# Kernel optimization log

Measured on AMD Instinct MI355X. Metric: run time of the kernel, lower is better.

## Reference

```python
import jax, jax.numpy as jnp
import numpy as np

B, T, C = 2, 2048, 1024
NH = 16

def setup_inputs() -> dict:
    key = jax.random.key(0)
    ks = jax.random.split(key, 5)
    s = 0.02
    return {
        "x": jax.random.normal(ks[0], (B, T, C), dtype=jnp.float32),
        "w_attn": jax.random.normal(ks[1], (C, 3 * C), dtype=jnp.float32) * s,
        "b_attn": jax.random.normal(ks[2], (3 * C,), dtype=jnp.float32) * s,
        "w_proj": jax.random.normal(ks[3], (C, C), dtype=jnp.float32) * s,
        "b_proj": jax.random.normal(ks[4], (C,), dtype=jnp.float32) * s,
        "n_heads": NH,
    }

def reference(x, w_attn, b_attn, w_proj, b_proj, n_heads):
    Bx, Tx, Cx = x.shape
    hd = Cx // n_heads
    qkv = x @ w_attn + b_attn                      # [B,T,3C]
    q, k, v = jnp.split(qkv, 3, axis=-1)
    # [B,T,H,hd] -> [B,H,T,hd]
    q = q.reshape(Bx, Tx, n_heads, hd).transpose(0, 2, 1, 3)
    k = k.reshape(Bx, Tx, n_heads, hd).transpose(0, 2, 1, 3)
    v = v.reshape(Bx, Tx, n_heads, hd).transpose(0, 2, 1, 3)
    scale = 1.0 / np.sqrt(hd).astype(np.float32)
    att = jnp.einsum('bhqd,bhkd->bhqk', q, k) * scale   # [B,H,T,T]
    causal = jnp.tril(jnp.ones((Tx, Tx), dtype=bool))
    att = jnp.where(causal[None, None], att, -jnp.inf)
    att = jax.nn.softmax(att, axis=-1)
    y = jnp.einsum('bhqk,bhkd->bhqd', att, v)            # [B,H,T,hd]
    y = y.transpose(0, 2, 1, 3).reshape(Bx, Tx, Cx)
    return y @ w_proj + b_proj
```

## Files before the change

### kernel.cpp

```cpp
#include <hip/hip_runtime.h>

typedef __bf16 bf16x8 __attribute__((ext_vector_type(8)));
typedef __bf16 bf16x4 __attribute__((ext_vector_type(4)));
typedef float  f32x4  __attribute__((ext_vector_type(4)));

#define MFMA_BF16(a, b, c) __builtin_amdgcn_mfma_f32_16x16x32_bf16((a), (b), (c), 0, 0, 0)
#define NEG_INF (-1e30f)
#define SCL 0.18033688f

__device__ __forceinline__ void gld16(const void* g, void* l) {
  __builtin_amdgcn_global_load_lds(
      (const __attribute__((address_space(1))) void*)g,
      (__attribute__((address_space(3))) void*)l, 16, 0, 0);
}

__global__ void cast_f32_bf16(const float* __restrict__ in,
                              __bf16* __restrict__ out, int n) {
  int i = (blockIdx.x * 256 + threadIdx.x) * 8;
  if (i >= n) return;
  float4 a = *(const float4*)&in[i];
  float4 b = *(const float4*)&in[i + 4];
  bf16x8 v;
  v[0] = (__bf16)a.x; v[1] = (__bf16)a.y; v[2] = (__bf16)a.z; v[3] = (__bf16)a.w;
  v[4] = (__bf16)b.x; v[5] = (__bf16)b.y; v[6] = (__bf16)b.z; v[7] = (__bf16)b.w;
  *(bf16x8*)&out[i] = v;
}

__global__ void transpose_f32_bf16(const float* __restrict__ in,
                                   __bf16* __restrict__ out, int R, int C) {
  __shared__ float t[32][33];
  int tx = threadIdx.x & 31, ty = threadIdx.x >> 5;
  int x = blockIdx.x * 32 + tx;
  int y0 = blockIdx.y * 32 + ty;
#pragma unroll
  for (int i = 0; i < 4; ++i)
    t[ty + 8 * i][tx] = in[(size_t)(y0 + 8 * i) * C + x];
  __syncthreads();
  int x2 = blockIdx.y * 32 + tx;
#pragma unroll
  for (int i = 0; i < 4; ++i)
    out[(size_t)(blockIdx.x * 32 + ty + 8 * i) * R + x2] = (__bf16)t[tx][ty + 8 * i];
}

__global__ void transpose_v(const __bf16* __restrict__ qkv,
                            __bf16* __restrict__ vt) {
  __shared__ __bf16 t[32][33];
  int tx = threadIdx.x & 31, ty = threadIdx.x >> 5;
  int bh = blockIdx.z, b = bh >> 4, h = bh & 15;
  int t0 = blockIdx.x * 32, d0 = blockIdx.y * 32;
#pragma unroll
  for (int i = 0; i < 4; ++i)
    t[ty + 8 * i][tx] =
        qkv[(size_t)(b * 2048 + t0 + ty + 8 * i) * 3072 + 2048 + h * 64 + d0 + tx];
  __syncthreads();
#pragma unroll
  for (int i = 0; i < 4; ++i)
    vt[(size_t)(bh * 64 + d0 + ty + 8 * i) * 2048 + t0 + tx] = t[tx][ty + 8 * i];
}

#define BN 128
#define BK 64

template <int BMT, typename TC>
__global__ __launch_bounds__(256) void gemm_bt_bias(
    const __bf16* __restrict__ A, const __bf16* __restrict__ Bt,
    const float* __restrict__ bias, TC* __restrict__ Cmat,
    int M, int N, int K) {
  constexpr int NI = BMT / 32;
  __shared__ __align__(16) __bf16 As[BMT * BK];
  __shared__ __align__(16) __bf16 Bs[BN * BK];
  int tid = threadIdx.x;
  int wave = tid >> 6, lane = tid & 63;
  int l16 = lane & 15, quad = lane >> 4;
  int wm = wave >> 1, wn = wave & 1;
  int m0 = blockIdx.y * BMT, n0 = blockIdx.x * BN;

  f32x4 acc[NI][4];
#pragma unroll
  for (int i = 0; i < NI; ++i)
#pragma unroll
    for (int j = 0; j < 4; ++j) acc[i][j] = (f32x4){0.f, 0.f, 0.f, 0.f};

  int row = tid >> 3;
  int kc = ((tid & 7) ^ ((tid >> 3) & 7)) * 8;
  int xr = (l16 & 7) * 8;

  for (int k0 = 0; k0 < K; k0 += BK) {
#pragma unroll
    for (int i = 0; i < NI; ++i)
      gld16(&A[(size_t)(m0 + row + i * 32) * K + k0 + kc],
            (char*)As + (i * 256 + wave * 64) * 16);
#pragma unroll
    for (int j = 0; j < 4; ++j)
      gld16(&Bt[(size_t)(n0 + row + j * 32) * K + k0 + kc],
            (char*)Bs + (j * 256 + wave * 64) * 16);
    __syncthreads();
#pragma unroll
    for (int ks = 0; ks < 2; ++ks) {
      bf16x8 af[NI], bfr[4];
#pragma unroll
      for (int i = 0; i < NI; ++i)
        af[i] = *(const bf16x8*)&As[(wm * (BMT / 2) + i * 16 + l16) * BK +
                                    ((ks * 32 + quad * 8) ^ xr)];
#pragma unroll
      for (int j = 0; j < 4; ++j)
        bfr[j] = *(const bf16x8*)&Bs[(wn * 64 + j * 16 + l16) * BK +
                                     ((ks * 32 + quad * 8) ^ xr)];
#pragma unroll
      for (int i = 0; i < NI; ++i)
#pragma unroll
        for (int j = 0; j < 4; ++j) acc[i][j] = MFMA_BF16(af[i], bfr[j], acc[i][j]);
    }
    __syncthreads();
  }
#pragma unroll
  for (int i = 0; i < NI; ++i) {
#pragma unroll
    for (int j = 0; j < 4; ++j) {
      int col = n0 + wn * 64 + j * 16 + l16;
      float bv = bias[col];
#pragma unroll
      for (int r = 0; r < 4; ++r) {
        int rw = m0 + wm * (BMT / 2) + i * 16 + quad * 4 + r;
        Cmat[(size_t)rw * N + col] = (TC)(acc[i][j][r] + bv);
      }
    }
  }
}

__global__ __launch_bounds__(256) void attn_causal(
    const __bf16* __restrict__ qkv, const __bf16* __restrict__ vt,
    __bf16* __restrict__ y) {
  __shared__ __align__(16) __bf16 Kb[2][64 * 64];
  __shared__ __align__(16) __bf16 Vb[2][64 * 64];
  __shared__ __align__(16) __bf16 Ps[4][16 * 72];
  const int tid = threadIdx.x;
  const int wave = tid >> 6, lane = tid & 63;
  const int l16 = lane & 15, quad = lane >> 4;
  const int bh = blockIdx.x;
  const int b = bh >> 4, h = bh & 15;
  const int RS = 3072;

  const int row0 = tid >> 3;
  const int kcs = ((tid & 7) ^ ((tid >> 3) & 7)) * 8;
  const int xr = (l16 & 7) * 8;
  const __bf16* kbase = qkv + (size_t)(b * 2048) * RS + 1024 + h * 64 + kcs;
  const __bf16* vbase = vt + (size_t)(bh * 64) * 2048 + kcs;

#pragma unroll 1
  for (int phase = 0; phase < 2; ++phase) {
    const int qt = phase ? (31 - (int)blockIdx.y) : (int)blockIdx.y;

    int qrow = b * 2048 + qt * 64 + wave * 16 + l16;
    const __bf16* qbase = qkv + (size_t)qrow * RS + h * 64;
    bf16x8 qf0 = *(const bf16x8*)(qbase + quad * 8);
    bf16x8 qf1 = *(const bf16x8*)(qbase + 32 + quad * 8);

    float l_i = 0.f;
    f32x4 o[4];
#pragma unroll
    for (int j = 0; j < 4; ++j) o[j] = (f32x4){0.f, 0.f, 0.f, 0.f};

#pragma unroll
    for (int i = 0; i < 2; ++i) {
      gld16(kbase + (size_t)(row0 + 32 * i) * RS,
            (char*)Kb[0] + (i * 256 + tid) * 16);
      gld16(vbase + (size_t)(row0 + 32 * i) * 2048,
            (char*)Vb[0] + (i * 256 + tid) * 16);
    }
    __syncthreads();

    for (int kt = 0; kt <= qt; ++kt) {
      const int cur = kt & 1;
      if (kt < qt) {
#pragma unroll
        for (int i = 0; i < 2; ++i) {
          gld16(kbase + (size_t)((kt + 1) * 64 + row0 + 32 * i) * RS,
                (char*)Kb[cur ^ 1] + (i * 256 + tid) * 16);
          gld16(vbase + (size_t)(row0 + 32 * i) * 2048 + (kt + 1) * 64,
                (char*)Vb[cur ^ 1] + (i * 256 + tid) * 16);
        }
      }

      f32x4 s[4];
#pragma unroll
      for (int j = 0; j < 4; ++j) s[j] = (f32x4){0.f, 0.f, 0.f, 0.f};
#pragma unroll
      for (int j = 0; j < 4; ++j) {
        bf16x8 kf0 = *(const bf16x8*)&Kb[cur][(j * 16 + l16) * 64 + ((quad * 8) ^ xr)];
        bf16x8 kf1 = *(const bf16x8*)&Kb[cur][(j * 16 + l16) * 64 + ((32 + quad * 8) ^ xr)];
        s[j] = MFMA_BF16(kf0, qf0, s[j]);
        s[j] = MFMA_BF16(kf1, qf1, s[j]);
      }

      if (kt == qt) {
        int qg = wave * 16 + l16;
#pragma unroll
        for (int j = 0; j < 4; ++j)
#pragma unroll
          for (int r = 0; r < 4; ++r)
            if (j * 16 + quad * 4 + r > qg) s[j][r] = NEG_INF;
      }

#pragma unroll
      for (int j = 0; j < 4; ++j) {
        bf16x4 pb;
#pragma unroll
        for (int r = 0; r < 4; ++r) {
          float p = __builtin_amdgcn_exp2f(s[j][r] * SCL);
          l_i += p;
          pb[r] = (__bf16)p;
        }
        *(bf16x4*)&Ps[wave][l16 * 72 + j * 16 + quad * 4] = pb;
      }

#pragma unroll
      for (int ks = 0; ks < 2; ++ks) {
        bf16x8 pf = *(const bf16x8*)&Ps[wave][l16 * 72 + ks * 32 + quad * 8];
#pragma unroll
        for (int j = 0; j < 4; ++j) {
          bf16x8 vf = *(const bf16x8*)&Vb[cur][(j * 16 + l16) * 64 +
                                              ((ks * 32 + quad * 8) ^ xr)];
          o[j] = MFMA_BF16(pf, vf, o[j]);
        }
      }
      __syncthreads();
    }

    float lred = l_i;
    lred += __shfl_xor(lred, 16);
    lred += __shfl_xor(lred, 32);
    int orow = b * 2048 + qt * 64 + wave * 16 + quad * 4;
#pragma unroll
    for (int r = 0; r < 4; ++r) {
      float inv = 1.f / __shfl(lred, quad * 4 + r);
#pragma unroll
      for (int j = 0; j < 4; ++j)
        y[(size_t)(orow + r) * 1024 + h * 64 + j * 16 + l16] = (__bf16)(o[j][r] * inv);
    }
  }
}

extern "C" void kernel_launch(void* const* d_in, const int* in_sizes, int n_in,
                              void* d_out, int out_size, void* d_ws, size_t ws_size,
                              hipStream_t stream) {
  (void)in_sizes; (void)n_in; (void)out_size; (void)ws_size;
  const float* x      = (const float*)d_in[0];
  const float* w_attn = (const float*)d_in[1];
  const float* b_attn = (const float*)d_in[2];
  const float* w_proj = (const float*)d_in[3];
  const float* b_proj = (const float*)d_in[4];
  float* out = (float*)d_out;

  __bf16* wt_attn = (__bf16*)d_ws;
  __bf16* wt_proj = wt_attn + (size_t)3072 * 1024;
  __bf16* qkv     = wt_proj + (size_t)1024 * 1024;
  __bf16* ybuf    = qkv + (size_t)4096 * 3072;
  __bf16* vtbuf   = ybuf + (size_t)4096 * 1024;

  cast_f32_bf16<<<4096 * 1024 / 2048, 256, 0, stream>>>(x, ybuf, 4096 * 1024);

  transpose_f32_bf16<<<dim3(3072 / 32, 1024 / 32), 256, 0, stream>>>(w_attn, wt_attn, 1024, 3072);
  transpose_f32_bf16<<<dim3(1024 / 32, 1024 / 32), 256, 0, stream>>>(w_proj, wt_proj, 1024, 1024);

  gemm_bt_bias<128, __bf16><<<dim3(3072 / BN, 4096 / 128), 256, 0, stream>>>(
      ybuf, wt_attn, b_attn, qkv, 4096, 3072, 1024);

  transpose_v<<<dim3(64, 2, 32), 256, 0, stream>>>(qkv, vtbuf);

  attn_causal<<<dim3(2 * 16, 16), 256, 0, stream>>>(qkv, vtbuf, ybuf);

  gemm_bt_bias<64, float><<<dim3(1024 / BN, 4096 / 64), 256, 0, stream>>>(
      ybuf, wt_proj, b_proj, out, 4096, 1024, 1024);
}
```

Baseline: 179.5 us.

## Process two 16-row query tiles per wave in attention with 128-thread blocks

The causal attention kernel now runs 2 waves per block instead of 4, and each wave handles 32 query rows as two 16-row tiles. Each K and V fragment read from shared memory feeds two MFMAs, which halves LDS reads per unit of compute, and the K/V tile loads are spread over 4 iterations per thread. The cost is more accumulator registers per wave and half as many waves per CU, so there is less latency hiding on a grid that only has 512 blocks.

```diff
diff --git a/kernel.cpp b/kernel.cpp
--- a/kernel.cpp
+++ b/kernel.cpp
@@ -128,12 +128,12 @@
   }
 }
 
-__global__ __launch_bounds__(256) void attn_causal(
+__global__ __launch_bounds__(128) void attn_causal(
     const __bf16* __restrict__ qkv, const __bf16* __restrict__ vt,
     __bf16* __restrict__ y) {
   __shared__ __align__(16) __bf16 Kb[2][64 * 64];
   __shared__ __align__(16) __bf16 Vb[2][64 * 64];
-  __shared__ __align__(16) __bf16 Ps[4][16 * 72];
+  __shared__ __align__(16) __bf16 Ps[2][32 * 72];
   const int tid = threadIdx.x;
   const int wave = tid >> 6, lane = tid & 63;
   const int l16 = lane & 15, quad = lane >> 4;
@@ -151,22 +151,28 @@
   for (int phase = 0; phase < 2; ++phase) {
     const int qt = phase ? (31 - (int)blockIdx.y) : (int)blockIdx.y;
 
-    int qrow = b * 2048 + qt * 64 + wave * 16 + l16;
-    const __bf16* qbase = qkv + (size_t)qrow * RS + h * 64;
-    bf16x8 qf0 = *(const bf16x8*)(qbase + quad * 8);
-    bf16x8 qf1 = *(const bf16x8*)(qbase + 32 + quad * 8);
-
-    float l_i = 0.f;
-    f32x4 o[4];
-#pragma unroll
-    for (int j = 0; j < 4; ++j) o[j] = (f32x4){0.f, 0.f, 0.f, 0.f};
-
-#pragma unroll
-    for (int i = 0; i < 2; ++i) {
-      gld16(kbase + (size_t)(row0 + 32 * i) * RS,
-            (char*)Kb[0] + (i * 256 + tid) * 16);
-      gld16(vbase + (size_t)(row0 + 32 * i) * 2048,
-            (char*)Vb[0] + (i * 256 + tid) * 16);
+    bf16x8 qf[2][2];
+#pragma unroll
+    for (int t = 0; t < 2; ++t) {
+      int qrow = b * 2048 + qt * 64 + wave * 32 + t * 16 + l16;
+      const __bf16* qbase = qkv + (size_t)qrow * RS + h * 64;
+      qf[t][0] = *(const bf16x8*)(qbase + quad * 8);
+      qf[t][1] = *(const bf16x8*)(qbase + 32 + quad * 8);
+    }
+
+    float l_i[2] = {0.f, 0.f};
+    f32x4 o[2][4];
+#pragma unroll
+    for (int t = 0; t < 2; ++t)
+#pragma unroll
+      for (int j = 0; j < 4; ++j) o[t][j] = (f32x4){0.f, 0.f, 0.f, 0.f};
+
+#pragma unroll
+    for (int i = 0; i < 4; ++i) {
+      gld16(kbase + (size_t)(row0 + 16 * i) * RS,
+            (char*)Kb[0] + (i * 128 + tid) * 16);
+      gld16(vbase + (size_t)(row0 + 16 * i) * 2048,
+            (char*)Vb[0] + (i * 128 + tid) * 16);
     }
     __syncthreads();
 
@@ -174,69 +180,87 @@
       const int cur = kt & 1;
       if (kt < qt) {
 #pragma unroll
-        for (int i = 0; i < 2; ++i) {
-          gld16(kbase + (size_t)((kt + 1) * 64 + row0 + 32 * i) * RS,
-                (char*)Kb[cur ^ 1] + (i * 256 + tid) * 16);
-          gld16(vbase + (size_t)(row0 + 32 * i) * 2048 + (kt + 1) * 64,
-                (char*)Vb[cur ^ 1] + (i * 256 + tid) * 16);
-        }
-      }
-
-      f32x4 s[4];
-#pragma unroll
-      for (int j = 0; j < 4; ++j) s[j] = (f32x4){0.f, 0.f, 0.f, 0.f};
+        for (int i = 0; i < 4; ++i) {
+          gld16(kbase + (size_t)((kt + 1) * 64 + row0 + 16 * i) * RS,
+                (char*)Kb[cur ^ 1] + (i * 128 + tid) * 16);
+          gld16(vbase + (size_t)(row0 + 16 * i) * 2048 + (kt + 1) * 64,
+                (char*)Vb[cur ^ 1] + (i * 128 + tid) * 16);
+        }
+      }
+
+      f32x4 s[2][4];
+#pragma unroll
+      for (int t = 0; t < 2; ++t)
+#pragma unroll
+        for (int j = 0; j < 4; ++j) s[t][j] = (f32x4){0.f, 0.f, 0.f, 0.f};
 #pragma unroll
       for (int j = 0; j < 4; ++j) {
         bf16x8 kf0 = *(const bf16x8*)&Kb[cur][(j * 16 + l16) * 64 + ((quad * 8) ^ xr)];
         bf16x8 kf1 = *(const bf16x8*)&Kb[cur][(j * 16 + l16) * 64 + ((32 + quad * 8) ^ xr)];
-        s[j] = MFMA_BF16(kf0, qf0, s[j]);
-        s[j] = MFMA_BF16(kf1, qf1, s[j]);
+#pragma unroll
+        for (int t = 0; t < 2; ++t) {
+          s[t][j] = MFMA_BF16(kf0, qf[t][0], s[t][j]);
+          s[t][j] = MFMA_BF16(kf1, qf[t][1], s[t][j]);
+        }
       }
 
       if (kt == qt) {
-        int qg = wave * 16 + l16;
-#pragma unroll
-        for (int j = 0; j < 4; ++j)
-#pragma unroll
-          for (int r = 0; r < 4; ++r)
-            if (j * 16 + quad * 4 + r > qg) s[j][r] = NEG_INF;
-      }
-
-#pragma unroll
-      for (int j = 0; j < 4; ++j) {
-        bf16x4 pb;
-#pragma unroll
-        for (int r = 0; r < 4; ++r) {
-          float p = __builtin_amdgcn_exp2f(s[j][r] * SCL);
-          l_i += p;
-          pb[r] = (__bf16)p;
-        }
-        *(bf16x4*)&Ps[wave][l16 * 72 + j * 16 + quad * 4] = pb;
-      }
+#pragma unroll
+        for (int t = 0; t < 2; ++t) {
+          int qg = wave * 32 + t * 16 + l16;
+#pragma unroll
+          for (int j = 0; j < 4; ++j)
+#pragma unroll
+            for (int r = 0; r < 4; ++r)
+              if (j * 16 + quad * 4 + r > qg) s[t][j][r] = NEG_INF;
+        }
+      }
+
+#pragma unroll
+      for (int t = 0; t < 2; ++t)
+#pragma unroll
+        for (int j = 0; j < 4; ++j) {
+          bf16x4 pb;
+#pragma unroll
+          for (int r = 0; r < 4; ++r) {
+            float p = __builtin_amdgcn_exp2f(s[t][j][r] * SCL);
+            l_i[t] += p;
+            pb[r] = (__bf16)p;
+          }
+          *(bf16x4*)&Ps[wave][(t * 16 + l16) * 72 + j * 16 + quad * 4] = pb;
+        }
 
 #pragma unroll
       for (int ks = 0; ks < 2; ++ks) {
-        bf16x8 pf = *(const bf16x8*)&Ps[wave][l16 * 72 + ks * 32 + quad * 8];
+        bf16x8 pf[2];
+#pragma unroll
+        for (int t = 0; t < 2; ++t)
+          pf[t] = *(const bf16x8*)&Ps[wave][(t * 16 + l16) * 72 + ks * 32 + quad * 8];
 #pragma unroll
         for (int j = 0; j < 4; ++j) {
           bf16x8 vf = *(const bf16x8*)&Vb[cur][(j * 16 + l16) * 64 +
                                               ((ks * 32 + quad * 8) ^ xr)];
-          o[j] = MFMA_BF16(pf, vf, o[j]);
+#pragma unroll
+          for (int t = 0; t < 2; ++t) o[t][j] = MFMA_BF16(pf[t], vf, o[t][j]);
         }
       }
       __syncthreads();
     }
 
-    float lred = l_i;
-    lred += __shfl_xor(lred, 16);
-    lred += __shfl_xor(lred, 32);
-    int orow = b * 2048 + qt * 64 + wave * 16 + quad * 4;
-#pragma unroll
-    for (int r = 0; r < 4; ++r) {
-      float inv = 1.f / __shfl(lred, quad * 4 + r);
-#pragma unroll
-      for (int j = 0; j < 4; ++j)
-        y[(size_t)(orow + r) * 1024 + h * 64 + j * 16 + l16] = (__bf16)(o[j][r] * inv);
+#pragma unroll
+    for (int t = 0; t < 2; ++t) {
+      float lred = l_i[t];
+      lred += __shfl_xor(lred, 16);
+      lred += __shfl_xor(lred, 32);
+      int orow = b * 2048 + qt * 64 + wave * 32 + t * 16 + quad * 4;
+#pragma unroll
+      for (int r = 0; r < 4; ++r) {
+        float inv = 1.f / __shfl(lred, quad * 4 + r);
+#pragma unroll
+        for (int j = 0; j < 4; ++j)
+          y[(size_t)(orow + r) * 1024 + h * 64 + j * 16 + l16] =
+              (__bf16)(o[t][j][r] * inv);
+      }
     }
   }
 }
@@ -268,7 +292,7 @@
 
   transpose_v<<<dim3(64, 2, 32), 256, 0, stream>>>(qkv, vtbuf);
 
-  attn_causal<<<dim3(2 * 16, 16), 256, 0, stream>>>(qkv, vtbuf, ybuf);
+  attn_causal<<<dim3(2 * 16, 16), 128, 0, stream>>>(qkv, vtbuf, ybuf);
 
   gemm_bt_bias<64, float><<<dim3(1024 / BN, 4096 / 64), 256, 0, stream>>>(
       ybuf, wt_proj, b_proj, out, 4096, 1024, 1024);
```

New measurement: 194.4 us. 1.08x slower.
